# Kernel tuning notes

Measured on AMD Instinct MI355X. Metric: run time of the kernel, lower is better.

The kernel has to match this reference:

```python
import jax, jax.numpy as jnp
import numpy as np

B_, NWIN, WH, WW = 8, 256, 8, 8
DIM, HEADS = 192, 6
N = WH * WW


def setup_inputs() -> dict:
    key = jax.random.key(0)
    ks = jax.random.split(key, 5)
    return {
        "x": jax.random.normal(ks[0], (B_, NWIN, N, DIM), dtype=jnp.float32),
        "qkv_w": jax.random.normal(ks[1], (3 * DIM, DIM), dtype=jnp.float32) * 0.02,
        "qkv_b": jax.random.normal(ks[2], (3 * DIM,), dtype=jnp.float32) * 0.02,
        "proj_w": jax.random.normal(ks[3], (DIM, DIM), dtype=jnp.float32) * 0.02,
        "proj_b": jax.random.normal(ks[4], (DIM,), dtype=jnp.float32) * 0.02,
    }


def _grad_magnitude(t, B, H, n, d, Wh, Ww):
    # t: [B,H,n,N,d] -> spatial layout [B,H,n,d,Wh,Ww]
    t = jnp.swapaxes(t, 3, 4).reshape(B, H, n, d, Wh, Ww)
    # forward finite difference with zero pre-pad (matches conv2d [-1,1] pad=1 then slice)
    gx = t - jnp.concatenate([jnp.zeros_like(t[..., :1]), t[..., :-1]], axis=-1)
    gy = t - jnp.concatenate([jnp.zeros_like(t[..., :1, :]), t[..., :-1, :]], axis=-2)
    return jnp.sum(jnp.abs(gx) + jnp.abs(gy), axis=(-1, -2))  # [B,H,n,d]


def reference(x, qkv_w, qkv_b, proj_w, proj_b):
    B, n, Ntok, C = x.shape
    H = HEADS
    d = C // H
    scale = d ** (-0.5)
    qkv = x @ qkv_w.T + qkv_b                       # [B,n,N,3C]
    qkv = qkv.reshape(B, n, Ntok, 3, H, d)
    qkv = jnp.transpose(qkv, (3, 0, 4, 1, 2, 5))    # [3,B,H,n,N,d]
    q, k, v = qkv[0] * scale, qkv[1], qkv[2]
    qg = _grad_magnitude(q, B, H, n, d, WH, WW)     # [B,H,n,d]
    kg = _grad_magnitude(k, B, H, n, d, WH, WW)
    qg = jnp.swapaxes(qg, 2, 3)[..., None]          # [B,H,d,n,1]
    kg = jnp.swapaxes(kg, 2, 3)[..., None]          # [B,H,d,n,1]
    attn = qg @ jnp.swapaxes(kg, -1, -2)            # [B,H,d,n,n] rank-1 scores
    attn = jax.nn.softmax(attn, axis=-1)
    vp = jnp.transpose(v, (0, 1, 4, 2, 3))          # [B,H,d,n,N]
    out = attn @ vp                                 # [B,H,d,n,N]
    out = jnp.transpose(out, (0, 3, 4, 1, 2)).reshape(B * n, Ntok, C)
    return out @ proj_w.T + proj_b                  # [B*n, N, C]
```

## Files before the change

### kernel.cpp

```cpp
#include <hip/hip_runtime.h>
#include <cstddef>


#define SCALE 0.17677669529663687f

typedef __attribute__((ext_vector_type(8))) short short8;
typedef __attribute__((ext_vector_type(4))) float f32x4;

__device__ __forceinline__ unsigned short f2bf(float f) {
    unsigned u = __float_as_uint(f);
    u += 0x7fffu + ((u >> 16) & 1u);
    return (unsigned short)(u >> 16);
}
__device__ __forceinline__ float bf2f(unsigned int h) {
    return __uint_as_float(h << 16);
}
__device__ __forceinline__ unsigned pack2(unsigned short a, unsigned short b) {
    return (unsigned)a | ((unsigned)b << 16);
}

__global__ __launch_bounds__(256) void wsplit_kernel(
    const float* __restrict__ w, unsigned short* __restrict__ Wh,
    unsigned short* __restrict__ Wl)
{
    int idx = blockIdx.x * 256 + threadIdx.x;
    float v = w[idx];
    unsigned short h = f2bf(v);
    Wh[idx] = h;
    if (idx < 73728) Wl[idx] = f2bf(v - bf2f(h));
}

__global__ __launch_bounds__(256) void wproj_kernel(
    const float* __restrict__ w, unsigned short* __restrict__ Wp)
{
    int idx = blockIdx.x * 256 + threadIdx.x;
    Wp[idx] = f2bf(w[idx]);
}

__global__ __launch_bounds__(256, 3) void qkv_fused_kernel(
    const float* __restrict__ x, const unsigned short* __restrict__ Wh,
    const unsigned short* __restrict__ Wl, const float* __restrict__ bias,
    unsigned short* __restrict__ vT, float* __restrict__ qg, float* __restrict__ kg)
{
    __shared__ unsigned short As_h[6 * 2048];
    __shared__ unsigned short As_l[6 * 2048];

    const int tid = threadIdx.x;
    const int wq = tid >> 6, lane = tid & 63;
    const int quad = lane >> 4, col = lane & 15;
    const int gw = blockIdx.x;
    const int b = gw >> 8, win = gw & 255;
    const int m0 = gw * 64;

    {
        const int arow = tid >> 2;
        const int apart = tid & 3;
        const float* xp = x + (size_t)(m0 + arow) * 192 + apart * 8;
        const int slot = (arow >> 4) * 512 + apart * 128 + (arow & 15) * 8;
        float4 va[6], vb[6];
#pragma unroll
        for (int kk = 0; kk < 6; ++kk) {
            va[kk] = *(const float4*)(xp + kk * 32);
            vb[kk] = *(const float4*)(xp + kk * 32 + 4);
        }
#pragma unroll
        for (int kk = 0; kk < 6; ++kk) {
            float v[8] = {va[kk].x, va[kk].y, va[kk].z, va[kk].w,
                          vb[kk].x, vb[kk].y, vb[kk].z, vb[kk].w};
            unsigned short h[8], l[8];
#pragma unroll
            for (int i = 0; i < 8; ++i) {
                h[i] = f2bf(v[i]);
                l[i] = f2bf(v[i] - bf2f(h[i]));
            }
            uint4 H = make_uint4(pack2(h[0], h[1]), pack2(h[2], h[3]),
                                 pack2(h[4], h[5]), pack2(h[6], h[7]));
            uint4 L = make_uint4(pack2(l[0], l[1]), pack2(l[2], l[3]),
                                 pack2(l[4], l[5]), pack2(l[6], l[7]));
            *(uint4*)&As_h[kk * 2048 + slot] = H;
            *(uint4*)&As_l[kk * 2048 + slot] = L;
        }
    }
    __syncthreads();

    const unsigned short* wh_base = Wh + (size_t)(wq * 16 + col) * 192 + quad * 8;
    const unsigned short* wl_base = Wl + (size_t)(wq * 16 + col) * 192 + quad * 8;

#pragma unroll
    for (int g = 0; g < 3; ++g) {
        const bool qk = (g < 2);

        f32x4 acc[3][4];
#pragma unroll
        for (int js = 0; js < 3; ++js)
#pragma unroll
            for (int mi = 0; mi < 4; ++mi) {
                f32x4 z = {0.f, 0.f, 0.f, 0.f};
                acc[js][mi] = z;
            }

        uint4 cbh[3], cbl[3], nbh[3], nbl[3];
#pragma unroll
        for (int js = 0; js < 3; ++js) {
            const int s = g * 3 + js;
            cbh[js] = *(const uint4*)(wh_base + (size_t)s * 12288);
            if (qk) cbl[js] = *(const uint4*)(wl_base + (size_t)s * 12288);
        }

#pragma unroll
        for (int kk = 0; kk < 6; ++kk) {
            if (kk < 5) {
#pragma unroll
                for (int js = 0; js < 3; ++js) {
                    const int s = g * 3 + js;
                    nbh[js] = *(const uint4*)(wh_base + (size_t)s * 12288 + (kk + 1) * 32);
                    if (qk) nbl[js] = *(const uint4*)(wl_base + (size_t)s * 12288 + (kk + 1) * 32);
                }
            }
            short8 ah[4], al[4];
#pragma unroll
            for (int mi = 0; mi < 4; ++mi) {
                ah[mi] = *(const short8*)&As_h[kk * 2048 + mi * 512 + lane * 8];
                if (qk) al[mi] = *(const short8*)&As_l[kk * 2048 + mi * 512 + lane * 8];
            }
#pragma unroll
            for (int js = 0; js < 3; ++js) {
                short8 bh = *(const short8*)&cbh[js];
                if (qk) {
                    short8 bl = *(const short8*)&cbl[js];
#pragma unroll
                    for (int mi = 0; mi < 4; ++mi) {
                        acc[js][mi] = __builtin_amdgcn_mfma_f32_16x16x32_bf16(al[mi], bh, acc[js][mi], 0, 0, 0);
                        acc[js][mi] = __builtin_amdgcn_mfma_f32_16x16x32_bf16(ah[mi], bl, acc[js][mi], 0, 0, 0);
                        acc[js][mi] = __builtin_amdgcn_mfma_f32_16x16x32_bf16(ah[mi], bh, acc[js][mi], 0, 0, 0);
                    }
                } else {
#pragma unroll
                    for (int mi = 0; mi < 4; ++mi)
                        acc[js][mi] = __builtin_amdgcn_mfma_f32_16x16x32_bf16(ah[mi], bh, acc[js][mi], 0, 0, 0);
                }
            }
#pragma unroll
            for (int js = 0; js < 3; ++js) {
                cbh[js] = nbh[js];
                if (qk) cbl[js] = nbl[js];
            }
        }

        if (g < 2) {
#pragma unroll
            for (int js = 0; js < 3; ++js) {
                const int s = g * 3 + js;
                const int n = wq + s * 4;
                const float bv = bias[n * 16 + col];
#pragma unroll
                for (int mi = 0; mi < 4; ++mi)
#pragma unroll
                    for (int r = 0; r < 4; ++r)
                        acc[js][mi][r] += bv;

                float yx[4][4], p3[4];
#pragma unroll
                for (int mi = 0; mi < 4; ++mi) {
#pragma unroll
                    for (int r = 0; r < 4; ++r)
                        yx[mi][r] = __shfl_xor(acc[js][mi][r], 32);
                    p3[mi] = __shfl_xor(acc[js][mi][3], 16);
                }
                float sum = 0.f;
#pragma unroll
                for (int mi = 0; mi < 4; ++mi)
#pragma unroll
                    for (int r = 0; r < 4; ++r) {
                        float v = acc[js][mi][r];
                        float gx = (r > 0) ? (v - acc[js][mi][r - 1])
                                           : ((quad & 1) ? (v - p3[mi]) : v);
                        float gy = (quad >= 2) ? (v - yx[mi][r])
                                               : ((mi > 0) ? (v - yx[mi - 1][r]) : v);
                        sum += fabsf(gx) + fabsf(gy);
                    }
                sum += __shfl_xor(sum, 16);
                sum += __shfl_xor(sum, 32);
                float* dst = (g == 0) ? qg : kg;
                const int chb = ((g == 0) ? n : n - 12) * 16;
                const float sc = (g == 0) ? SCALE : 1.0f;
                if (lane < 16)
                    dst[(size_t)(b * 192 + chb + lane) * 256 + win] = sum * sc;
            }
        } else {
#pragma unroll
            for (int js = 0; js < 3; ++js) {
                const int s = 6 + js;
                const int n = wq + s * 4;
                const float bv = bias[n * 16 + col];
                const int ch = (n - 24) * 16 + col;
#pragma unroll
                for (int mi = 0; mi < 4; ++mi) {
                    int tok0 = mi * 16 + quad * 4;
                    ushort4 o = make_ushort4(f2bf(acc[js][mi][0] + bv),
                                             f2bf(acc[js][mi][1] + bv),
                                             f2bf(acc[js][mi][2] + bv),
                                             f2bf(acc[js][mi][3] + bv));
                    *(ushort4*)(vT + (size_t)(b * 192 + ch) * 16384 + win * 64 + tok0) = o;
                }
            }
        }
    }
}

__global__ __launch_bounds__(256) void attn_mfma_kernel(
    const unsigned short* __restrict__ vT, const float* __restrict__ qg,
    const float* __restrict__ kg, unsigned short* __restrict__ attbuf)
{
    __shared__ unsigned short Vs[64 * 264];
    __shared__ float kds[256];
    __shared__ float red[256];

    const int g = blockIdx.x;
    const int tid = threadIdx.x;
    const int wave = tid >> 6, lane = tid & 63;
    const int quad = lane >> 4, col = lane & 15;

    float kv = kg[(size_t)g * 256 + tid];
    red[tid] = kv;
    __syncthreads();
    for (int s = 128; s > 0; s >>= 1) {
        if (tid < s) red[tid] = fmaxf(red[tid], red[tid + s]);
        __syncthreads();
    }
    kds[tid] = kv - red[0];

    const unsigned short* vb = vT + (size_t)g * 16384;
    {
        const int jr = tid >> 3;
        const int tb = (tid & 7) * 8;
#pragma unroll
        for (int it = 0; it < 8; ++it) {
            int j = it * 32 + jr;
            uint4 u = *(const uint4*)(vb + (size_t)j * 64 + tb);
            Vs[(tb + 0) * 264 + j] = (unsigned short)(u.x & 0xffffu);
            Vs[(tb + 1) * 264 + j] = (unsigned short)(u.x >> 16);
            Vs[(tb + 2) * 264 + j] = (unsigned short)(u.y & 0xffffu);
            Vs[(tb + 3) * 264 + j] = (unsigned short)(u.y >> 16);
            Vs[(tb + 4) * 264 + j] = (unsigned short)(u.z & 0xffffu);
            Vs[(tb + 5) * 264 + j] = (unsigned short)(u.z >> 16);
            Vs[(tb + 6) * 264 + j] = (unsigned short)(u.w & 0xffffu);
            Vs[(tb + 7) * 264 + j] = (unsigned short)(u.w >> 16);
        }
    }

    float ai[4];
#pragma unroll
    for (int mi = 0; mi < 4; ++mi)
        ai[mi] = qg[(size_t)g * 256 + wave * 64 + mi * 16 + col];

    __syncthreads();

    f32x4 acc[4][4];
#pragma unroll
    for (int mi = 0; mi < 4; ++mi)
#pragma unroll
        for (int ni = 0; ni < 4; ++ni) {
            f32x4 z = {0.f, 0.f, 0.f, 0.f};
            acc[mi][ni] = z;
        }
    float den[4] = {0.f, 0.f, 0.f, 0.f};

    for (int kt = 0; kt < 8; ++kt) {
        const int k0 = kt * 32;
        float4 ka = *(const float4*)&kds[k0 + quad * 8];
        float4 kb = *(const float4*)&kds[k0 + quad * 8 + 4];
        float kv8[8] = {ka.x, ka.y, ka.z, ka.w, kb.x, kb.y, kb.z, kb.w};

        short8 bfr[4];
#pragma unroll
        for (int ni = 0; ni < 4; ++ni)
            bfr[ni] = *(const short8*)&Vs[(ni * 16 + col) * 264 + k0 + quad * 8];

#pragma unroll
        for (int mi = 0; mi < 4; ++mi) {
            short8 ef;
            float dl = 0.f;
#pragma unroll
            for (int j = 0; j < 8; ++j) {
                float e = __expf(ai[mi] * kv8[j]);
                unsigned short h = f2bf(e);
                ef[j] = (short)h;
                dl += bf2f(h);
            }
            den[mi] += dl;
#pragma unroll
            for (int ni = 0; ni < 4; ++ni)
                acc[mi][ni] = __builtin_amdgcn_mfma_f32_16x16x32_bf16(
                    ef, bfr[ni], acc[mi][ni], 0, 0, 0);
        }
    }

#pragma unroll
    for (int mi = 0; mi < 4; ++mi) {
        den[mi] += __shfl_xor(den[mi], 16);
        den[mi] += __shfl_xor(den[mi], 32);
    }

    unsigned short* ob = attbuf + (size_t)g * 16384;
#pragma unroll
    for (int mi = 0; mi < 4; ++mi) {
        float invr[4];
#pragma unroll
        for (int r = 0; r < 4; ++r)
            invr[r] = 1.0f / __shfl(den[mi], quad * 4 + r);
#pragma unroll
        for (int ni = 0; ni < 4; ++ni)
#pragma unroll
            for (int r = 0; r < 4; ++r) {
                int i = wave * 64 + mi * 16 + quad * 4 + r;
                int tok = ni * 16 + col;
                ob[i * 64 + tok] = f2bf(acc[mi][ni][r] * invr[r]);
            }
    }
}

__global__ __launch_bounds__(256) void proj_mfma_kernel(
    const unsigned short* __restrict__ attbuf, const unsigned short* __restrict__ Wp,
    const float* __restrict__ bias, float* __restrict__ out)
{
    __shared__ unsigned short Bs[64 * 40];
    __shared__ float T[32 * 197];

    const int tid = threadIdx.x;
    const int wave = tid >> 6, lane = tid & 63;
    const int quad = lane >> 4, col = lane & 15;
    const int rowg0 = blockIdx.x * 64;
    const int b = rowg0 >> 14;
    const int rl0 = rowg0 & 16383;
    const unsigned short* ab = attbuf + (size_t)b * 3145728;

    f32x4 acc[3][4];
#pragma unroll
    for (int mi = 0; mi < 3; ++mi)
#pragma unroll
        for (int ni = 0; ni < 4; ++ni) {
            f32x4 z = {0.f, 0.f, 0.f, 0.f};
            acc[mi][ni] = z;
        }

    const int chl = tid >> 3;
    const int rb = (tid & 7) * 8;

    for (int kt = 0; kt < 6; ++kt) {
        __syncthreads();
        {
            uint4 u = *(const uint4*)(ab + (size_t)(kt * 32 + chl) * 16384 + rl0 + rb);
            Bs[(rb + 0) * 40 + chl] = (unsigned short)(u.x & 0xffffu);
            Bs[(rb + 1) * 40 + chl] = (unsigned short)(u.x >> 16);
            Bs[(rb + 2) * 40 + chl] = (unsigned short)(u.y & 0xffffu);
            Bs[(rb + 3) * 40 + chl] = (unsigned short)(u.y >> 16);
            Bs[(rb + 4) * 40 + chl] = (unsigned short)(u.z & 0xffffu);
            Bs[(rb + 5) * 40 + chl] = (unsigned short)(u.z >> 16);
            Bs[(rb + 6) * 40 + chl] = (unsigned short)(u.w & 0xffffu);
            Bs[(rb + 7) * 40 + chl] = (unsigned short)(u.w >> 16);
        }
        __syncthreads();

        short8 bfr[4], af[3];
#pragma unroll
        for (int ni = 0; ni < 4; ++ni)
            bfr[ni] = *(const short8*)&Bs[(ni * 16 + col) * 40 + quad * 8];
#pragma unroll
        for (int mi = 0; mi < 3; ++mi)
            af[mi] = *(const short8*)(Wp + (size_t)(wave * 48 + mi * 16 + col) * 192
                                      + kt * 32 + quad * 8);
#pragma unroll
        for (int mi = 0; mi < 3; ++mi)
#pragma unroll
            for (int ni = 0; ni < 4; ++ni)
                acc[mi][ni] = __builtin_amdgcn_mfma_f32_16x16x32_bf16(
                    af[mi], bfr[ni], acc[mi][ni], 0, 0, 0);
    }

    float br[3][4];
#pragma unroll
    for (int mi = 0; mi < 3; ++mi)
#pragma unroll
        for (int r = 0; r < 4; ++r)
            br[mi][r] = bias[wave * 48 + mi * 16 + quad * 4 + r];

#pragma unroll
    for (int h = 0; h < 2; ++h) {
        __syncthreads();
#pragma unroll
        for (int nh = 0; nh < 2; ++nh) {
            int ni = h * 2 + nh;
#pragma unroll
            for (int mi = 0; mi < 3; ++mi)
#pragma unroll
                for (int r = 0; r < 4; ++r)
                    T[(nh * 16 + col) * 197 + wave * 48 + mi * 16 + quad * 4 + r] =
                        acc[mi][ni][r] + br[mi][r];
        }
        __syncthreads();
        {
            int row = tid >> 3;
            int ck = (tid & 7) * 24;
            float* op = out + (size_t)(rowg0 + h * 32 + row) * 192 + ck;
#pragma unroll
            for (int q4 = 0; q4 < 6; ++q4) {
                float4 o = make_float4(T[row * 197 + ck + q4 * 4 + 0],
                                       T[row * 197 + ck + q4 * 4 + 1],
                                       T[row * 197 + ck + q4 * 4 + 2],
                                       T[row * 197 + ck + q4 * 4 + 3]);
                *(float4*)(op + q4 * 4) = o;
            }
        }
    }
}

extern "C" void kernel_launch(void* const* d_in, const int* in_sizes, int n_in,
                              void* d_out, int out_size, void* d_ws, size_t ws_size,
                              hipStream_t stream) {
    const float* x      = (const float*)d_in[0];
    const float* qkv_w  = (const float*)d_in[1];
    const float* qkv_b  = (const float*)d_in[2];
    const float* proj_w = (const float*)d_in[3];
    const float* proj_b = (const float*)d_in[4];
    float* out = (float*)d_out;

    unsigned short* base16 = (unsigned short*)d_ws;
    unsigned short* vT16   = base16;
    unsigned short* attbuf = base16 + 25165824;
    float* qg = (float*)(base16 + 50331648);
    float* kg = qg + 393216;
    unsigned short* Wh = (unsigned short*)(kg + 393216);
    unsigned short* Wl = Wh + 110592;
    unsigned short* Wp = Wl + 73728;

    wsplit_kernel<<<432, 256, 0, stream>>>(qkv_w, Wh, Wl);
    wproj_kernel<<<144, 256, 0, stream>>>(proj_w, Wp);
    qkv_fused_kernel<<<2048, 256, 0, stream>>>(x, Wh, Wl, qkv_b, vT16, qg, kg);
    attn_mfma_kernel<<<1536, 256, 0, stream>>>(vT16, qg, kg, attbuf);
    proj_mfma_kernel<<<2048, 256, 0, stream>>>(attbuf, Wp, proj_b, out);
}
```

Before: 351.0 us.

## Stream x tiles through double-buffered LDS and remap blocks across XCDs

Replaces the full 6-chunk LDS staging of the converted x tile with a 2-slot double buffer that is refilled per k-chunk, reloading and reconverting x from global memory for each of the three output groups. The smaller LDS footprint allows raising launch bounds to 4 blocks per CU, and the block index is remapped so each XCD handles a contiguous range of windows. The cost is three times more x global loads and bf16 split conversions, plus an extra barrier per k-step, in exchange for higher occupancy and overlap of loads with MFMA work.

After: 403.1 us. 14.8% more time.

```diff
diff --git a/kernel.cpp b/kernel.cpp
--- a/kernel.cpp
+++ b/kernel.cpp
@@ -37,58 +37,63 @@
     Wp[idx] = f2bf(w[idx]);
 }
 
-__global__ __launch_bounds__(256, 3) void qkv_fused_kernel(
+__global__ __launch_bounds__(256, 4) void qkv_fused_kernel(
     const float* __restrict__ x, const unsigned short* __restrict__ Wh,
     const unsigned short* __restrict__ Wl, const float* __restrict__ bias,
     unsigned short* __restrict__ vT, float* __restrict__ qg, float* __restrict__ kg)
 {
-    __shared__ unsigned short As_h[6 * 2048];
-    __shared__ unsigned short As_l[6 * 2048];
+    __shared__ unsigned short Ah[2][2048];
+    __shared__ unsigned short Al[2][2048];
 
     const int tid = threadIdx.x;
     const int wq = tid >> 6, lane = tid & 63;
     const int quad = lane >> 4, col = lane & 15;
-    const int gw = blockIdx.x;
-    const int b = gw >> 8, win = gw & 255;
-    const int m0 = gw * 64;
-
-    {
-        const int arow = tid >> 2;
-        const int apart = tid & 3;
-        const float* xp = x + (size_t)(m0 + arow) * 192 + apart * 8;
-        const int slot = (arow >> 4) * 512 + apart * 128 + (arow & 15) * 8;
-        float4 va[6], vb[6];
-#pragma unroll
-        for (int kk = 0; kk < 6; ++kk) {
-            va[kk] = *(const float4*)(xp + kk * 32);
-            vb[kk] = *(const float4*)(xp + kk * 32 + 4);
-        }
-#pragma unroll
-        for (int kk = 0; kk < 6; ++kk) {
-            float v[8] = {va[kk].x, va[kk].y, va[kk].z, va[kk].w,
-                          vb[kk].x, vb[kk].y, vb[kk].z, vb[kk].w};
-            unsigned short h[8], l[8];
-#pragma unroll
-            for (int i = 0; i < 8; ++i) {
-                h[i] = f2bf(v[i]);
-                l[i] = f2bf(v[i] - bf2f(h[i]));
-            }
-            uint4 H = make_uint4(pack2(h[0], h[1]), pack2(h[2], h[3]),
-                                 pack2(h[4], h[5]), pack2(h[6], h[7]));
-            uint4 L = make_uint4(pack2(l[0], l[1]), pack2(l[2], l[3]),
-                                 pack2(l[4], l[5]), pack2(l[6], l[7]));
-            *(uint4*)&As_h[kk * 2048 + slot] = H;
-            *(uint4*)&As_l[kk * 2048 + slot] = L;
-        }
-    }
-    __syncthreads();
+    const int bid = blockIdx.x;
+    const int xcd = bid & 7;
+    const int i2 = bid >> 3;
+    const int b = i2 & 7;
+    const int win = xcd * 32 + (i2 >> 3);
+    const int m0 = (b * 256 + win) * 64;
+
+    const int arow = tid >> 2;
+    const int apart = tid & 3;
+    const float* xp = x + (size_t)(m0 + arow) * 192 + apart * 8;
+    const int slot = (arow >> 4) * 512 + apart * 128 + (arow & 15) * 8;
 
     const unsigned short* wh_base = Wh + (size_t)(wq * 16 + col) * 192 + quad * 8;
     const unsigned short* wl_base = Wl + (size_t)(wq * 16 + col) * 192 + quad * 8;
 
+    float4 SA[2], SB[2];
+    auto xload = [&](int kk, int s) {
+        SA[s] = *(const float4*)(xp + kk * 32);
+        SB[s] = *(const float4*)(xp + kk * 32 + 4);
+    };
+    auto cwrite = [&](int kk, int s) {
+        float v[8] = {SA[s].x, SA[s].y, SA[s].z, SA[s].w,
+                      SB[s].x, SB[s].y, SB[s].z, SB[s].w};
+        unsigned short h[8], l[8];
+#pragma unroll
+        for (int i = 0; i < 8; ++i) {
+            h[i] = f2bf(v[i]);
+            l[i] = f2bf(v[i] - bf2f(h[i]));
+        }
+        uint4 H = make_uint4(pack2(h[0], h[1]), pack2(h[2], h[3]),
+                             pack2(h[4], h[5]), pack2(h[6], h[7]));
+        uint4 L = make_uint4(pack2(l[0], l[1]), pack2(l[2], l[3]),
+                             pack2(l[4], l[5]), pack2(l[6], l[7]));
+        *(uint4*)&Ah[kk & 1][slot] = H;
+        *(uint4*)&Al[kk & 1][slot] = L;
+    };
+
 #pragma unroll
     for (int g = 0; g < 3; ++g) {
         const bool qk = (g < 2);
+
+        xload(0, 0);
+        xload(1, 1);
+        __syncthreads();
+        cwrite(0, 0);
+        xload(2, 0);
 
         f32x4 acc[3][4];
 #pragma unroll
@@ -106,9 +111,20 @@
             cbh[js] = *(const uint4*)(wh_base + (size_t)s * 12288);
             if (qk) cbl[js] = *(const uint4*)(wl_base + (size_t)s * 12288);
         }
+        __syncthreads();
 
 #pragma unroll
         for (int kk = 0; kk < 6; ++kk) {
+            short8 ah[4], al[4];
+#pragma unroll
+            for (int mi = 0; mi < 4; ++mi) {
+                ah[mi] = *(const short8*)&Ah[kk & 1][mi * 512 + lane * 8];
+                if (qk) al[mi] = *(const short8*)&Al[kk & 1][mi * 512 + lane * 8];
+            }
+            if (kk < 5) cwrite(kk + 1, (kk + 1) & 1);
+            if (kk < 3) xload(kk + 3, (kk + 1) & 1);
+            __syncthreads();
+
             if (kk < 5) {
 #pragma unroll
                 for (int js = 0; js < 3; ++js) {
@@ -116,12 +132,6 @@
                     nbh[js] = *(const uint4*)(wh_base + (size_t)s * 12288 + (kk + 1) * 32);
                     if (qk) nbl[js] = *(const uint4*)(wl_base + (size_t)s * 12288 + (kk + 1) * 32);
                 }
-            }
-            short8 ah[4], al[4];
-#pragma unroll
-            for (int mi = 0; mi < 4; ++mi) {
-                ah[mi] = *(const short8*)&As_h[kk * 2048 + mi * 512 + lane * 8];
-                if (qk) al[mi] = *(const short8*)&As_l[kk * 2048 + mi * 512 + lane * 8];
             }
 #pragma unroll
             for (int js = 0; js < 3; ++js) {
```
